# Kernel optimization log

Measured on AMD Instinct MI355X. Metric: run time of the kernel, lower is better.

Reference implementation:

```python
import jax, jax.numpy as jnp
import numpy as np

N_EXPERT = 8
TOP_K = 2
NEG_INF = -1e9  # finite sentinel so softmax grads stay well-defined


def setup_inputs() -> dict:
    key = jax.random.key(0)
    ks = jax.random.split(key, 8)
    B, S, D, F, E = 2, 2048, 1024, 4096, N_EXPERT
    sd = 1.0 / np.sqrt(D)
    sf = 1.0 / np.sqrt(F)
    return {
        "x": jax.random.normal(ks[0], (B, S, D), jnp.float32),
        "noise": jax.random.normal(ks[1], (B, S, E), jnp.float32),
        "Wr": jax.random.normal(ks[2], (D, E), jnp.float32) * sd,
        "br": jnp.zeros((E,), jnp.float32),
        "Wn": jax.random.normal(ks[3], (D, E), jnp.float32) * sd,
        "bn": jnp.zeros((E,), jnp.float32),
        "W1": jax.random.normal(ks[4], (E, D, F), jnp.float32) * sd,
        "b1": jnp.zeros((E, F), jnp.float32),
        "W2": jax.random.normal(ks[5], (E, F, D), jnp.float32) * sf,
        "b2": jnp.zeros((E, D), jnp.float32),
    }


def reference(x, noise, Wr, br, Wn, bn, W1, b1, W2, b2):
    # NoisyTopkRouter: logits + noise * softplus(noise_logits)
    logits = jnp.einsum("bsd,de->bse", x, Wr) + br
    noise_logits = jnp.einsum("bsd,de->bse", x, Wn) + bn
    noisy = logits + noise * jax.nn.softplus(noise_logits)

    # keep only top-k logits, -inf elsewhere, softmax over experts
    _, top_ids = jax.lax.top_k(noisy, TOP_K)                  # [B,S,K]
    sel = jnp.sum(jax.nn.one_hot(top_ids, N_EXPERT, dtype=noisy.dtype), axis=-2) > 0  # [B,S,E]
    gates = jax.nn.softmax(jnp.where(sel, noisy, NEG_INF), axis=-1)  # zeros off top-k

    # Expert MLP: Linear -> ReLU -> Linear (dropout = 0 at inference).
    # Gates are exactly zero for non-selected experts, so the dense einsum
    # combine equals the original masked gather/scatter-add.
    h = jax.nn.relu(jnp.einsum("bsd,edf->ebsf", x, W1) + b1[:, None, None, :])
    eo = jnp.einsum("ebsf,efd->ebsd", h, W2) + b2[:, None, None, :]
    return jnp.einsum("bse,ebsd->bsd", gates, eo)
```

## Files before the change

kernel.cpp:

```cpp
#include <hip/hip_runtime.h>

#define T_TOK 4096
#define DDIM 1024
#define FDIM 4096
#define NE 8
#define NPAIR 8192
#define MAXT128 72

typedef short bf16x8 __attribute__((ext_vector_type(8)));
typedef float f32x4 __attribute__((ext_vector_type(4)));

__device__ inline unsigned short f2bf(float f) {
  union { float f; unsigned u; } a; a.f = f;
  unsigned r = a.u + 0x7fffu + ((a.u >> 16) & 1u);
  return (unsigned short)(r >> 16);
}

__device__ __forceinline__ void gload16(const void* g, void* l) {
  __builtin_amdgcn_global_load_lds(
      (const __attribute__((address_space(1))) unsigned int*)g,
      (__attribute__((address_space(3))) unsigned int*)l, 16, 0, 0);
}

__global__ __launch_bounds__(256) void router_kernel(
    const float* __restrict__ x, const float* __restrict__ noise,
    const float* __restrict__ Wr, const float* __restrict__ br,
    const float* __restrict__ Wn, const float* __restrict__ bn,
    int* __restrict__ tok_top, float* __restrict__ tok_gate)
{
  int t = blockIdx.x * 4 + (threadIdx.x >> 6);
  int lane = threadIdx.x & 63;
  const float* xr = x + (size_t)t * DDIM;
  float accR[NE] = {}, accN[NE] = {};
  for (int d = lane; d < DDIM; d += 64) {
    float xv = xr[d];
    const float* wr = Wr + (size_t)d * NE;
    const float* wn = Wn + (size_t)d * NE;
#pragma unroll
    for (int e = 0; e < NE; ++e) {
      accR[e] = fmaf(xv, wr[e], accR[e]);
      accN[e] = fmaf(xv, wn[e], accN[e]);
    }
  }
#pragma unroll
  for (int off = 32; off > 0; off >>= 1) {
#pragma unroll
    for (int e = 0; e < NE; ++e) {
      accR[e] += __shfl_xor(accR[e], off);
      accN[e] += __shfl_xor(accN[e], off);
    }
  }
  if (lane == 0) {
    float noisy[NE];
#pragma unroll
    for (int e = 0; e < NE; ++e) {
      float lg = accR[e] + br[e];
      float nl = accN[e] + bn[e];
      float sp = fmaxf(nl, 0.f) + log1pf(expf(-fabsf(nl)));
      noisy[e] = lg + noise[(size_t)t * NE + e] * sp;
    }
    int e0 = 0;
#pragma unroll
    for (int e = 1; e < NE; ++e) if (noisy[e] > noisy[e0]) e0 = e;
    int e1 = (e0 == 0) ? 1 : 0;
#pragma unroll
    for (int e = 0; e < NE; ++e)
      if (e != e0 && e != e1 && noisy[e] > noisy[e1]) e1 = e;
    float v0 = noisy[e0], v1 = noisy[e1];
    float ex = __expf(v1 - v0);
    float inv = 1.f / (1.f + ex);
    tok_top[t * 2] = e0; tok_top[t * 2 + 1] = e1;
    tok_gate[t * 2] = inv; tok_gate[t * 2 + 1] = ex * inv;
  }
}

__global__ __launch_bounds__(256) void scan_scatter_kernel(
    const int* __restrict__ tok_top, int* __restrict__ off, int* __restrict__ tiles,
    int* __restrict__ pair_tok, int* __restrict__ tok_ppos)
{
  __shared__ int scnt[NE], scur[NE];
  int tid = threadIdx.x;
  if (tid < NE) scnt[tid] = 0;
  __syncthreads();
  for (int t = tid; t < T_TOK; t += 256) {
    atomicAdd(&scnt[tok_top[2 * t]], 1);
    atomicAdd(&scnt[tok_top[2 * t + 1]], 1);
  }
  __syncthreads();
  if (tid == 0) {
    int s = 0, nt = 0;
    for (int e = 0; e < NE; ++e) {
      scur[e] = s; off[e] = s;
      int tt = (scnt[e] + 127) >> 7;
      for (int m = 0; m < tt; ++m) tiles[1 + nt++] = (e << 8) | m;
      s += scnt[e];
    }
    off[NE] = s;
    tiles[0] = nt;
  }
  __syncthreads();
  for (int t = tid; t < T_TOK; t += 256) {
#pragma unroll
    for (int k = 0; k < 2; ++k) {
      int e = tok_top[2 * t + k];
      int pos = atomicAdd(&scur[e], 1);
      pair_tok[pos] = t;
      tok_ppos[2 * t + k] = pos;
    }
  }
}

__global__ __launch_bounds__(256) void gather_x_kernel(
    const float* __restrict__ x, const int* __restrict__ pair_tok,
    ushort* __restrict__ xg)
{
  int p = blockIdx.x;
  int t = pair_tok[p];
  int tid = threadIdx.x;
  float4 v = ((const float4*)(x + (size_t)t * DDIM))[tid];
  ushort4 o;
  o.x = f2bf(v.x); o.y = f2bf(v.y); o.z = f2bf(v.z); o.w = f2bf(v.w);
  ((ushort4*)(xg + (size_t)p * DDIM))[tid] = o;
}

__global__ __launch_bounds__(256) void transpose_bf_kernel(
    const float* __restrict__ W1, const float* __restrict__ W2,
    ushort* __restrict__ WT1, ushort* __restrict__ WT2)
{
  __shared__ float tile[64][65];
  int z = blockIdx.z;
  const float* src; ushort* dst; int R, C, bx, by;
  if (z < NE) {
    src = W1 + (size_t)z * DDIM * FDIM; dst = WT1 + (size_t)z * FDIM * DDIM;
    R = DDIM; C = FDIM; bx = blockIdx.x; by = blockIdx.y;
  } else {
    src = W2 + (size_t)(z - NE) * FDIM * DDIM; dst = WT2 + (size_t)(z - NE) * DDIM * FDIM;
    R = FDIM; C = DDIM; bx = blockIdx.y; by = blockIdx.x;
  }
  int c0 = bx * 64, r0 = by * 64;
  int tid = threadIdx.x;
  int tr = tid >> 4;
  int tc4 = (tid & 15) * 4;
#pragma unroll
  for (int i = 0; i < 64; i += 16) {
    float4 v = *(const float4*)(src + (size_t)(r0 + tr + i) * C + c0 + tc4);
    tile[tr + i][tc4] = v.x; tile[tr + i][tc4 + 1] = v.y;
    tile[tr + i][tc4 + 2] = v.z; tile[tr + i][tc4 + 3] = v.w;
  }
  __syncthreads();
  int cc = tid >> 4;
  int rr4 = (tid & 15) * 4;
#pragma unroll
  for (int i = 0; i < 64; i += 16) {
    int c = cc + i;
    ushort4 o;
    o.x = f2bf(tile[rr4][c]); o.y = f2bf(tile[rr4 + 1][c]);
    o.z = f2bf(tile[rr4 + 2][c]); o.w = f2bf(tile[rr4 + 3][c]);
    *(ushort4*)(dst + (size_t)(c0 + c) * R + r0 + rr4) = o;
  }
}

template<int KD, int ND, int EPI>
__global__ __launch_bounds__(256) void gemm4_kernel(
    const ushort* __restrict__ A, const ushort* __restrict__ BT,
    const int* __restrict__ off, const int* __restrict__ tiles,
    const float* __restrict__ bias,
    ushort* __restrict__ Hout, float* __restrict__ EOout)
{
  constexpr int GX = ND / 128;
  constexpr int NKT = KD / 32;
  __shared__ __align__(16) ushort As[128 * 32];
  __shared__ __align__(16) ushort Bs[128 * 32];

  int total = tiles[0] * GX;
  int orig = blockIdx.x + GX * (int)blockIdx.y;
  if (orig >= total) return;
  int q = total >> 3, r = total & 7, xcd = orig & 7, idx = orig >> 3;
  int wg = (xcd < r ? xcd * (q + 1) : r * (q + 1) + (xcd - r) * q) + idx;
  int ti = wg / GX, bx = wg - ti * GX;

  int te = tiles[1 + ti];
  int e = te >> 8, mt = te & 255;
  int base = off[e];
  int cnt = off[e + 1] - base;
  int m0 = mt << 7, n0 = bx << 7;

  int tid = threadIdx.x, lane = tid & 63, wid = tid >> 6;
  int wr = wid >> 1, wc = wid & 1;

  const char* Agb = (const char*)(A + (size_t)(base + m0) * KD);
  const char* Bgb = (const char*)(BT + ((size_t)e * ND + n0) * KD);

  f32x4 acc[4][4] = {};

  for (int t = 0; t < NKT; ++t) {
    __syncthreads();
    size_t kb = (size_t)t * 64;
#pragma unroll
    for (int c = 0; c < 2; ++c) {
      int ch = c * 256 + tid;
      int row = ch >> 2, b = (ch & 3) * 16;
      gload16(Agb + (size_t)row * (KD * 2) + kb + (b ^ ((row & 3) << 4)),
              (char*)As + ch * 16);
    }
#pragma unroll
    for (int c = 0; c < 2; ++c) {
      int ch = c * 256 + tid;
      int row = ch >> 2, b = (ch & 3) * 16;
      gload16(Bgb + (size_t)row * (KD * 2) + kb + (b ^ ((row & 3) << 4)),
              (char*)Bs + ch * 16);
    }
    __syncthreads();

    bf16x8 af[4], bv[4];
#pragma unroll
    for (int m = 0; m < 4; ++m) {
      int row = wr * 64 + m * 16 + (lane & 15);
      af[m] = *(const bf16x8*)((const char*)As + row * 64 +
                               (((lane >> 4) * 16) ^ ((row & 3) << 4)));
    }
#pragma unroll
    for (int n = 0; n < 4; ++n) {
      int row = wc * 64 + n * 16 + (lane & 15);
      bv[n] = *(const bf16x8*)((const char*)Bs + row * 64 +
                               (((lane >> 4) * 16) ^ ((row & 3) << 4)));
    }
#pragma unroll
    for (int m = 0; m < 4; ++m)
#pragma unroll
      for (int n = 0; n < 4; ++n)
        acc[m][n] = __builtin_amdgcn_mfma_f32_16x16x32_bf16(af[m], bv[n], acc[m][n], 0, 0, 0);
  }

  float bvv[4];
#pragma unroll
  for (int n = 0; n < 4; ++n)
    bvv[n] = bias[(size_t)e * ND + n0 + wc * 64 + n * 16 + (lane & 15)];
  int rq = (lane >> 4) << 2;
#pragma unroll
  for (int m = 0; m < 4; ++m) {
#pragma unroll
    for (int qq = 0; qq < 4; ++qq) {
      int rr = m0 + wr * 64 + m * 16 + rq + qq;
      if (rr < cnt) {
#pragma unroll
        for (int n = 0; n < 4; ++n) {
          int col = n0 + wc * 64 + n * 16 + (lane & 15);
          float v = acc[m][n][qq] + bvv[n];
          if (EPI == 0) {
            v = fmaxf(v, 0.f);
            Hout[(size_t)(base + rr) * ND + col] = f2bf(v);
          } else {
            EOout[(size_t)(base + rr) * ND + col] = v;
          }
        }
      }
    }
  }
}

__global__ __launch_bounds__(256) void combine_kernel(
    const float* __restrict__ eo, const int* __restrict__ tok_ppos,
    const float* __restrict__ tok_gate, float* __restrict__ out)
{
  int t = blockIdx.x;
  int tid = threadIdx.x;
  int p0 = tok_ppos[t * 2], p1 = tok_ppos[t * 2 + 1];
  float g0 = tok_gate[t * 2], g1 = tok_gate[t * 2 + 1];
  float4 a = ((const float4*)(eo + (size_t)p0 * DDIM))[tid];
  float4 b = ((const float4*)(eo + (size_t)p1 * DDIM))[tid];
  float4 o;
  o.x = g0 * a.x + g1 * b.x;
  o.y = g0 * a.y + g1 * b.y;
  o.z = g0 * a.z + g1 * b.z;
  o.w = g0 * a.w + g1 * b.w;
  ((float4*)(out + (size_t)t * DDIM))[tid] = o;
}

extern "C" void kernel_launch(void* const* d_in, const int* in_sizes, int n_in,
                              void* d_out, int out_size, void* d_ws, size_t ws_size,
                              hipStream_t stream)
{
  const float* x     = (const float*)d_in[0];
  const float* noise = (const float*)d_in[1];
  const float* Wr    = (const float*)d_in[2];
  const float* br    = (const float*)d_in[3];
  const float* Wn    = (const float*)d_in[4];
  const float* bn    = (const float*)d_in[5];
  const float* W1    = (const float*)d_in[6];
  const float* b1    = (const float*)d_in[7];
  const float* W2    = (const float*)d_in[8];
  const float* b2    = (const float*)d_in[9];
  float* out = (float*)d_out;

  char* ws = (char*)d_ws;
  size_t o = 0;
  auto alloc = [&](size_t sz) {
    void* p = ws + o;
    o = (o + sz + 255) & ~(size_t)255;
    return p;
  };
  ushort* WT1 = (ushort*)alloc((size_t)NE * FDIM * DDIM * 2);
  ushort* WT2 = (ushort*)alloc((size_t)NE * DDIM * FDIM * 2);
  ushort* XG  = (ushort*)alloc((size_t)(NPAIR + 256) * DDIM * 2);
  ushort* H   = (ushort*)alloc((size_t)(NPAIR + 256) * FDIM * 2);
  float*  EO  = (float*)alloc((size_t)(NPAIR + 256) * DDIM * 4);
  int*    TOK_TOP  = (int*)alloc(T_TOK * 2 * 4);
  float*  TOK_GATE = (float*)alloc(T_TOK * 2 * 4);
  int*    TOK_PPOS = (int*)alloc(T_TOK * 2 * 4);
  int*    PAIR_TOK = (int*)alloc(NPAIR * 4);
  int*    OFF = (int*)alloc(64);
  int*    TILES = (int*)alloc((1 + MAXT128) * 4);

  router_kernel<<<T_TOK / 4, 256, 0, stream>>>(x, noise, Wr, br, Wn, bn,
                                               TOK_TOP, TOK_GATE);
  scan_scatter_kernel<<<1, 256, 0, stream>>>(TOK_TOP, OFF, TILES, PAIR_TOK, TOK_PPOS);
  gather_x_kernel<<<NPAIR, 256, 0, stream>>>(x, PAIR_TOK, XG);
  transpose_bf_kernel<<<dim3(64, 16, 16), 256, 0, stream>>>(W1, W2, WT1, WT2);
  gemm4_kernel<DDIM, FDIM, 0>
      <<<dim3(FDIM / 128, MAXT128), 256, 0, stream>>>(XG, WT1, OFF, TILES, b1, H, nullptr);
  gemm4_kernel<FDIM, DDIM, 1>
      <<<dim3(DDIM / 128, MAXT128), 256, 0, stream>>>(H, WT2, OFF, TILES, b2, nullptr, EO);
  combine_kernel<<<T_TOK, 256, 0, stream>>>(EO, TOK_PPOS, TOK_GATE, out);
}
```

Baseline: 346.9 us.

## Fuse x bf16 conversion into router, gather rows in GEMM, double K tile

```diff
diff --git a/kernel.cpp b/kernel.cpp
--- a/kernel.cpp
+++ b/kernel.cpp
@@ -26,14 +26,17 @@
     const float* __restrict__ x, const float* __restrict__ noise,
     const float* __restrict__ Wr, const float* __restrict__ br,
     const float* __restrict__ Wn, const float* __restrict__ bn,
-    int* __restrict__ tok_top, float* __restrict__ tok_gate)
+    int* __restrict__ tok_top, float* __restrict__ tok_gate,
+    ushort* __restrict__ xb)
 {
   int t = blockIdx.x * 4 + (threadIdx.x >> 6);
   int lane = threadIdx.x & 63;
   const float* xr = x + (size_t)t * DDIM;
+  ushort* xo = xb + (size_t)t * DDIM;
   float accR[NE] = {}, accN[NE] = {};
   for (int d = lane; d < DDIM; d += 64) {
     float xv = xr[d];
+    xo[d] = f2bf(xv);
     const float* wr = Wr + (size_t)d * NE;
     const float* wn = Wn + (size_t)d * NE;
 #pragma unroll
@@ -78,49 +81,49 @@
     const int* __restrict__ tok_top, int* __restrict__ off, int* __restrict__ tiles,
     int* __restrict__ pair_tok, int* __restrict__ tok_ppos)
 {
-  __shared__ int scnt[NE], scur[NE];
+  __shared__ int smat[NE][256];
+  __shared__ int tot[NE];
+  __shared__ int loff[NE];
   int tid = threadIdx.x;
-  if (tid < NE) scnt[tid] = 0;
+  int c[NE] = {};
+  for (int i = 0; i < 16; ++i) {
+    int t = tid * 16 + i;
+    int e0 = tok_top[2 * t], e1 = tok_top[2 * t + 1];
+#pragma unroll
+    for (int e = 0; e < NE; ++e) c[e] += (e0 == e) + (e1 == e);
+  }
+#pragma unroll
+  for (int e = 0; e < NE; ++e) smat[e][tid] = c[e];
   __syncthreads();
-  for (int t = tid; t < T_TOK; t += 256) {
-    atomicAdd(&scnt[tok_top[2 * t]], 1);
-    atomicAdd(&scnt[tok_top[2 * t + 1]], 1);
+  if (tid < NE) {
+    int s = 0;
+    for (int j = 0; j < 256; ++j) { int v = smat[tid][j]; smat[tid][j] = s; s += v; }
+    tot[tid] = s;
   }
   __syncthreads();
   if (tid == 0) {
     int s = 0, nt = 0;
     for (int e = 0; e < NE; ++e) {
-      scur[e] = s; off[e] = s;
-      int tt = (scnt[e] + 127) >> 7;
+      loff[e] = s; off[e] = s;
+      int tt = (tot[e] + 127) >> 7;
       for (int m = 0; m < tt; ++m) tiles[1 + nt++] = (e << 8) | m;
-      s += scnt[e];
+      s += tot[e];
     }
     off[NE] = s;
     tiles[0] = nt;
   }
   __syncthreads();
-  for (int t = tid; t < T_TOK; t += 256) {
+  for (int i = 0; i < 16; ++i) {
+    int t = tid * 16 + i;
 #pragma unroll
     for (int k = 0; k < 2; ++k) {
       int e = tok_top[2 * t + k];
-      int pos = atomicAdd(&scur[e], 1);
+      int pos = loff[e] + smat[e][tid];
+      smat[e][tid] = smat[e][tid] + 1;
       pair_tok[pos] = t;
       tok_ppos[2 * t + k] = pos;
     }
   }
-}
-
-__global__ __launch_bounds__(256) void gather_x_kernel(
-    const float* __restrict__ x, const int* __restrict__ pair_tok,
-    ushort* __restrict__ xg)
-{
-  int p = blockIdx.x;
-  int t = pair_tok[p];
-  int tid = threadIdx.x;
-  float4 v = ((const float4*)(x + (size_t)t * DDIM))[tid];
-  ushort4 o;
-  o.x = f2bf(v.x); o.y = f2bf(v.y); o.z = f2bf(v.z); o.w = f2bf(v.w);
-  ((ushort4*)(xg + (size_t)p * DDIM))[tid] = o;
 }
 
 __global__ __launch_bounds__(256) void transpose_bf_kernel(
@@ -160,17 +163,17 @@
   }
 }
 
-template<int KD, int ND, int EPI>
+template<int KD, int ND, int EPI, int INDIR>
 __global__ __launch_bounds__(256) void gemm4_kernel(
     const ushort* __restrict__ A, const ushort* __restrict__ BT,
     const int* __restrict__ off, const int* __restrict__ tiles,
-    const float* __restrict__ bias,
+    const int* __restrict__ pair_tok, const float* __restrict__ bias,
     ushort* __restrict__ Hout, float* __restrict__ EOout)
 {
   constexpr int GX = ND / 128;
-  constexpr int NKT = KD / 32;
-  __shared__ __align__(16) ushort As[128 * 32];
-  __shared__ __align__(16) ushort Bs[128 * 32];
+  constexpr int NKT = KD / 64;
+  __shared__ __align__(16) ushort As[128 * 64];
+  __shared__ __align__(16) ushort Bs[128 * 64];
 
   int total = tiles[0] * GX;
   int orig = blockIdx.x + GX * (int)blockIdx.y;
@@ -188,48 +191,64 @@
   int tid = threadIdx.x, lane = tid & 63, wid = tid >> 6;
   int wr = wid >> 1, wc = wid & 1;
 
-  const char* Agb = (const char*)(A + (size_t)(base + m0) * KD);
+  int arow[4];
+#pragma unroll
+  for (int c = 0; c < 4; ++c) {
+    int rl = (c * 256 + tid) >> 3;
+    int mr = m0 + rl; if (mr >= cnt) mr = cnt - 1;
+    arow[c] = INDIR ? pair_tok[base + mr] : base + mr;
+  }
+  const char* Ab = (const char*)A;
   const char* Bgb = (const char*)(BT + ((size_t)e * ND + n0) * KD);
 
   f32x4 acc[4][4] = {};
 
   for (int t = 0; t < NKT; ++t) {
     __syncthreads();
-    size_t kb = (size_t)t * 64;
-#pragma unroll
-    for (int c = 0; c < 2; ++c) {
+    int kb = t * 128;
+#pragma unroll
+    for (int c = 0; c < 4; ++c) {
       int ch = c * 256 + tid;
-      int row = ch >> 2, b = (ch & 3) * 16;
-      gload16(Agb + (size_t)row * (KD * 2) + kb + (b ^ ((row & 3) << 4)),
+      int row = ch >> 3, b = (ch & 7) * 16;
+      gload16(Ab + (size_t)arow[c] * (KD * 2) + kb + (b ^ ((row & 7) << 4)),
               (char*)As + ch * 16);
     }
 #pragma unroll
-    for (int c = 0; c < 2; ++c) {
+    for (int c = 0; c < 4; ++c) {
       int ch = c * 256 + tid;
-      int row = ch >> 2, b = (ch & 3) * 16;
-      gload16(Bgb + (size_t)row * (KD * 2) + kb + (b ^ ((row & 3) << 4)),
+      int row = ch >> 3, b = (ch & 7) * 16;
+      gload16(Bgb + (size_t)row * (KD * 2) + kb + (b ^ ((row & 7) << 4)),
               (char*)Bs + ch * 16);
     }
     __syncthreads();
 
-    bf16x8 af[4], bv[4];
+    bf16x8 af[4][2], bv[4][2];
 #pragma unroll
     for (int m = 0; m < 4; ++m) {
       int row = wr * 64 + m * 16 + (lane & 15);
-      af[m] = *(const bf16x8*)((const char*)As + row * 64 +
-                               (((lane >> 4) * 16) ^ ((row & 3) << 4)));
+      int sw = (row & 7) << 4;
+#pragma unroll
+      for (int ks = 0; ks < 2; ++ks)
+        af[m][ks] = *(const bf16x8*)((const char*)As + row * 128 +
+                                     ((ks * 64 + (lane >> 4) * 16) ^ sw));
     }
 #pragma unroll
     for (int n = 0; n < 4; ++n) {
       int row = wc * 64 + n * 16 + (lane & 15);
-      bv[n] = *(const bf16x8*)((const char*)Bs + row * 64 +
-                               (((lane >> 4) * 16) ^ ((row & 3) << 4)));
-    }
-#pragma unroll
-    for (int m = 0; m < 4; ++m)
-#pragma unroll
-      for (int n = 0; n < 4; ++n)
-        acc[m][n] = __builtin_amdgcn_mfma_f32_16x16x32_bf16(af[m], bv[n], acc[m][n], 0, 0, 0);
+      int sw = (row & 7) << 4;
+#pragma unroll
+      for (int ks = 0; ks < 2; ++ks)
+        bv[n][ks] = *(const bf16x8*)((const char*)Bs + row * 128 +
+                                     ((ks * 64 + (lane >> 4) * 16) ^ sw));
+    }
+#pragma unroll
+    for (int ks = 0; ks < 2; ++ks)
+#pragma unroll
+      for (int m = 0; m < 4; ++m)
+#pragma unroll
+        for (int n = 0; n < 4; ++n)
+          acc[m][n] = __builtin_amdgcn_mfma_f32_16x16x32_bf16(
+              af[m][ks], bv[n][ks], acc[m][n], 0, 0, 0);
   }
 
   float bvv[4];
@@ -302,24 +321,23 @@
   };
   ushort* WT1 = (ushort*)alloc((size_t)NE * FDIM * DDIM * 2);
   ushort* WT2 = (ushort*)alloc((size_t)NE * DDIM * FDIM * 2);
-  ushort* XG  = (ushort*)alloc((size_t)(NPAIR + 256) * DDIM * 2);
+  ushort* XB  = (ushort*)alloc((size_t)T_TOK * DDIM * 2);
   ushort* H   = (ushort*)alloc((size_t)(NPAIR + 256) * FDIM * 2);
   float*  EO  = (float*)alloc((size_t)(NPAIR + 256) * DDIM * 4);
   int*    TOK_TOP  = (int*)alloc(T_TOK * 2 * 4);
   float*  TOK_GATE = (float*)alloc(T_TOK * 2 * 4);
   int*    TOK_PPOS = (int*)alloc(T_TOK * 2 * 4);
-  int*    PAIR_TOK = (int*)alloc(NPAIR * 4);
+  int*    PAIR_TOK = (int*)alloc((NPAIR + 256) * 4);
   int*    OFF = (int*)alloc(64);
   int*    TILES = (int*)alloc((1 + MAXT128) * 4);
 
   router_kernel<<<T_TOK / 4, 256, 0, stream>>>(x, noise, Wr, br, Wn, bn,
-                                               TOK_TOP, TOK_GATE);
+                                               TOK_TOP, TOK_GATE, XB);
   scan_scatter_kernel<<<1, 256, 0, stream>>>(TOK_TOP, OFF, TILES, PAIR_TOK, TOK_PPOS);
-  gather_x_kernel<<<NPAIR, 256, 0, stream>>>(x, PAIR_TOK, XG);
   transpose_bf_kernel<<<dim3(64, 16, 16), 256, 0, stream>>>(W1, W2, WT1, WT2);
-  gemm4_kernel<DDIM, FDIM, 0>
-      <<<dim3(FDIM / 128, MAXT128), 256, 0, stream>>>(XG, WT1, OFF, TILES, b1, H, nullptr);
-  gemm4_kernel<FDIM, DDIM, 1>
-      <<<dim3(DDIM / 128, MAXT128), 256, 0, stream>>>(H, WT2, OFF, TILES, b2, nullptr, EO);
+  gemm4_kernel<DDIM, FDIM, 0, 1>
+      <<<dim3(FDIM / 128, MAXT128), 256, 0, stream>>>(XB, WT1, OFF, TILES, PAIR_TOK, b1, H, nullptr);
+  gemm4_kernel<FDIM, DDIM, 1, 0>
+      <<<dim3(DDIM / 128, MAXT128), 256, 0, stream>>>(H, WT2, OFF, TILES, PAIR_TOK, b2, nullptr, EO);
   combine_kernel<<<T_TOK, 256, 0, stream>>>(EO, TOK_PPOS, TOK_GATE, out);
 }
```

Measured after the change: 324.4 us. -6.5%, faster.
